# Kernel optimization log

Measured on AMD Instinct MI355X. Metric: run time of the kernel, lower is better.

## Reference

```python
import jax, jax.numpy as jnp
import numpy as np

B, M, D = 4, 2048, 1024


def setup_inputs() -> dict:
    key = jax.random.key(0)
    k1, k2, k3, k4 = jax.random.split(key, 4)
    x = jax.random.normal(k1, (B, M, D), dtype=jnp.float32)
    scale = 0.02
    wq = jax.random.normal(k2, (D, D), dtype=jnp.float32) * scale
    wk = jax.random.normal(k3, (D, D), dtype=jnp.float32) * scale
    wv = jax.random.normal(k4, (D, D), dtype=jnp.float32) * scale
    return {"x": x, "wq": wq, "wk": wk, "wv": wv}


def _rope_tables(m, d):
    # Faithful to source: phi = 10000 ** (-2*(i-1)/d)  (note the (i-1), incl. i=0)
    i = jnp.arange(d // 2, dtype=jnp.float32)
    phi = jnp.power(10000.0, -2.0 * (i - 1.0) / d)  # [d/2]
    pos = jnp.arange(m, dtype=jnp.float32)
    ang = pos[:, None] * phi[None, :]  # [m, d/2]
    return jnp.cos(ang), jnp.sin(ang)


def _apply_rope(t, cos, sin):
    # Original does t[pos] @ R[pos] (row-vector times rotation matrix):
    #   out_even =  t_even*cos + t_odd*sin
    #   out_odd  = -t_even*sin + t_odd*cos
    te = t[..., 0::2]  # [b, m, d/2]
    to = t[..., 1::2]
    oe = te * cos + to * sin
    oo = -te * sin + to * cos
    return jnp.stack([oe, oo], axis=-1).reshape(t.shape)


def reference(x, wq, wk, wv):
    b, m, d = x.shape
    q = x @ wq.T
    k = x @ wk.T
    v = x @ wv.T
    cos, sin = _rope_tables(m, d)
    qr = _apply_rope(q, cos, sin)
    kr = _apply_rope(k, cos, sin)
    # causal SDPA (dropout disabled for deterministic reference)
    scores = jnp.einsum('bqd,bkd->bqk', qr, kr) / jnp.sqrt(jnp.float32(d))
    causal = jnp.tril(jnp.ones((m, m), dtype=bool))
    scores = jnp.where(causal[None, :, :], scores, jnp.finfo(scores.dtype).min)
    attn = jax.nn.softmax(scores, axis=-1)
    return jnp.einsum('bqk,bkd->bqd', attn, v)
```

## Files before the change

### kernel.cpp

```cpp
#include <hip/hip_runtime.h>
#include <hip/hip_bf16.h>
#include <math.h>


typedef __bf16 bf16x8 __attribute__((ext_vector_type(8)));
typedef float  f32x4  __attribute__((ext_vector_type(4)));

__device__ __forceinline__ ushort f2bf(float f) {
    __hip_bfloat16 h = __float2bfloat16(f);
    return *reinterpret_cast<ushort*>(&h);
}

__device__ __forceinline__ void async_load16(const ushort* g, ushort* l) {
    __builtin_amdgcn_global_load_lds(
        (const __attribute__((address_space(1))) void*)g,
        (__attribute__((address_space(3))) void*)l, 16, 0, 0);
}

__global__ __launch_bounds__(256) void cvt_all_kernel(
    const float* __restrict__ x,  const float* __restrict__ wq,
    const float* __restrict__ wk, const float* __restrict__ wv,
    ushort* __restrict__ xb, ushort* __restrict__ wqb,
    ushort* __restrict__ wkb, ushort* __restrict__ wvb,
    float2* __restrict__ cs)
{
    const int t = blockIdx.y;
    if (t == 4) {
        const int idx = blockIdx.x * 256 + threadIdx.x;
        if (idx < 2048 * 512) {
            const int pos = idx >> 9, i = idx & 511;
            const float phi = powf(10000.0f, -2.0f * ((float)i - 1.0f) / 1024.0f);
            float s, c;
            sincosf((float)pos * phi, &s, &c);
            cs[idx] = make_float2(c, s);
        }
        return;
    }
    const float* in  = (t == 0) ? x  : (t == 1) ? wq  : (t == 2) ? wk  : wv;
    ushort*      out = (t == 0) ? xb : (t == 1) ? wqb : (t == 2) ? wkb : wvb;
    const int n4 = (t == 0) ? 2097152 : 262144;
    int i = blockIdx.x * blockDim.x + threadIdx.x;
    if (i < n4) {
        float4 f = ((const float4*)in)[i];
        ushort4 o;
        o.x = f2bf(f.x); o.y = f2bf(f.y); o.z = f2bf(f.z); o.w = f2bf(f.w);
        ((ushort4*)out)[i] = o;
    }
}

__device__ __forceinline__ void gemm128_core_sb(
    const ushort* __restrict__ A, const ushort* __restrict__ B,
    int lda, int ldb, int m0, int n0, int kIters,
    ushort* As, ushort* Bs, f32x4 acc[4][4])
{
    const int tid  = threadIdx.x;
    const int lane = tid & 63, wave = tid >> 6;
    const int wm = (wave >> 1) * 64, wn = (wave & 1) * 64;
    const int quad = lane >> 4, l16 = lane & 15;
    const int srow = lane >> 2, c = lane & 3;
    const int rr   = wave * 32 + srow;
    const int cc   = c ^ ((rr >> 1) & 3);
    const int scol = cc * 8;

    const ushort* ag0 = A + (size_t)(m0 + rr) * lda + scol;
    const ushort* bg0 = B + (size_t)(n0 + rr) * ldb + scol;
    const ushort* ag1 = ag0 + (size_t)16 * lda;
    const ushort* bg1 = bg0 + (size_t)16 * ldb;
    ushort* la0 = As + (wave * 32) * 32;
    ushort* la1 = la0 + 16 * 32;
    ushort* lb0 = Bs + (wave * 32) * 32;
    ushort* lb1 = lb0 + 16 * 32;

    for (int kt = 0; kt < kIters; ++kt) {
        const int k0 = kt * 32;
        async_load16(ag0 + k0, la0);
        async_load16(ag1 + k0, la1);
        async_load16(bg0 + k0, lb0);
        async_load16(bg1 + k0, lb1);
        __syncthreads();
        bf16x8 aF[4], bF[4];
#pragma unroll
        for (int i = 0; i < 4; ++i) {
            const int r = wm + i * 16 + l16;
            aF[i] = *(const bf16x8*)(As + r * 32 + ((quad ^ ((r >> 1) & 3)) * 8));
        }
#pragma unroll
        for (int j = 0; j < 4; ++j) {
            const int r = wn + j * 16 + l16;
            bF[j] = *(const bf16x8*)(Bs + r * 32 + ((quad ^ ((r >> 1) & 3)) * 8));
        }
#pragma unroll
        for (int i = 0; i < 4; ++i)
#pragma unroll
            for (int j = 0; j < 4; ++j)
                acc[i][j] = __builtin_amdgcn_mfma_f32_16x16x32_bf16(aF[i], bF[j], acc[i][j], 0, 0, 0);
        __syncthreads();
    }
}

__device__ __forceinline__ void gemm128_core_db(
    const ushort* __restrict__ A, const ushort* __restrict__ B,
    int lda, int ldb, int m0, int n0, int kIters,
    ushort* As, ushort* Bs, f32x4 acc[4][4])
{
    const int tid  = threadIdx.x;
    const int lane = tid & 63, wave = tid >> 6;
    const int wm = (wave >> 1) * 64, wn = (wave & 1) * 64;
    const int quad = lane >> 4, l16 = lane & 15;
    const int srow = lane >> 2, c = lane & 3;
    const int rr   = wave * 32 + srow;
    const int cc   = c ^ ((rr >> 1) & 3);
    const int scol = cc * 8;

    const ushort* ag0 = A + (size_t)(m0 + rr) * lda + scol;
    const ushort* bg0 = B + (size_t)(n0 + rr) * ldb + scol;
    const ushort* ag1 = ag0 + (size_t)16 * lda;
    const ushort* bg1 = bg0 + (size_t)16 * ldb;
    const int lofs = (wave * 32) * 32;

    async_load16(ag0, As + lofs);
    async_load16(ag1, As + lofs + 16 * 32);
    async_load16(bg0, Bs + lofs);
    async_load16(bg1, Bs + lofs + 16 * 32);
    __syncthreads();

    int cur = 0;
    for (int kt = 0; kt < kIters; ++kt) {
        if (kt + 1 < kIters) {
            const int k1 = (kt + 1) * 32;
            const int nb = (cur ^ 1) * 4096;
            async_load16(ag0 + k1, As + nb + lofs);
            async_load16(ag1 + k1, As + nb + lofs + 16 * 32);
            async_load16(bg0 + k1, Bs + nb + lofs);
            async_load16(bg1 + k1, Bs + nb + lofs + 16 * 32);
        }
        const ushort* as = As + cur * 4096;
        const ushort* bs = Bs + cur * 4096;
        bf16x8 aF[4], bF[4];
#pragma unroll
        for (int i = 0; i < 4; ++i) {
            const int r = wm + i * 16 + l16;
            aF[i] = *(const bf16x8*)(as + r * 32 + ((quad ^ ((r >> 1) & 3)) * 8));
        }
#pragma unroll
        for (int j = 0; j < 4; ++j) {
            const int r = wn + j * 16 + l16;
            bF[j] = *(const bf16x8*)(bs + r * 32 + ((quad ^ ((r >> 1) & 3)) * 8));
        }
#pragma unroll
        for (int i = 0; i < 4; ++i)
#pragma unroll
            for (int j = 0; j < 4; ++j)
                acc[i][j] = __builtin_amdgcn_mfma_f32_16x16x32_bf16(aF[i], bF[j], acc[i][j], 0, 0, 0);
        __syncthreads();
        cur ^= 1;
    }
}

#define ACC_INIT4(acc) \
    _Pragma("unroll") for (int i = 0; i < 4; ++i) \
    _Pragma("unroll") for (int j = 0; j < 4; ++j) \
    _Pragma("unroll") for (int r = 0; r < 4; ++r) acc[i][j][r] = 0.0f;

__global__ __launch_bounds__(256) void qkv_rope_kernel(
    const ushort* __restrict__ xb, const ushort* __restrict__ wq,
    const ushort* __restrict__ wk, const ushort* __restrict__ wv,
    const float2* __restrict__ cs,
    ushort* __restrict__ Qr, ushort* __restrict__ Kr, ushort* __restrict__ VT)
{
    __shared__ __attribute__((aligned(16))) ushort As[128 * 32];
    __shared__ __attribute__((aligned(16))) ushort Bs[128 * 32];
    const int m0 = blockIdx.x * 128;
    const int n0 = blockIdx.y * 128;
    const int z  = blockIdx.z;
    const ushort* W = (z == 0) ? wq : (z == 1) ? wk : wv;

    f32x4 acc[4][4];
    ACC_INIT4(acc)
    gemm128_core_sb(xb, W, 1024, 1024, m0, n0, 32, As, Bs, acc);

    const int lane = threadIdx.x & 63, wave = threadIdx.x >> 6;
    const int wm = (wave >> 1) * 64, wn = (wave & 1) * 64;
    const int quad = lane >> 4, l16 = lane & 15;

    if (z < 2) {
        ushort* out = (z == 0) ? Qr : Kr;
#pragma unroll
        for (int j = 0; j < 4; ++j) {
            const int n = n0 + wn + j * 16 + l16;
            const int iidx = n >> 1;
            const bool odd = n & 1;
#pragma unroll
            for (int i = 0; i < 4; ++i) {
                const int mbase = m0 + wm + i * 16 + quad * 4;
                const int pos0  = mbase & 2047;
                const float2* csp = cs + (size_t)pos0 * 512 + iidx;
#pragma unroll
                for (int r = 0; r < 4; ++r) {
                    const float2 sc = csp[(size_t)r * 512];
                    float v = acc[i][j][r];
                    float p = __shfl_xor(v, 1);
                    float o = odd ? (v * sc.x - p * sc.y) : (v * sc.x + p * sc.y);
                    out[(size_t)(mbase + r) * 1024 + n] = f2bf(o);
                }
            }
        }
    } else {
#pragma unroll
        for (int i = 0; i < 4; ++i) {
            const int mbase = m0 + wm + i * 16 + quad * 4;
            const int b = mbase >> 11, pos0 = mbase & 2047;
#pragma unroll
            for (int j = 0; j < 4; ++j) {
                const int n = n0 + wn + j * 16 + l16;
                ushort4 o;
                o.x = f2bf(acc[i][j][0]); o.y = f2bf(acc[i][j][1]);
                o.z = f2bf(acc[i][j][2]); o.w = f2bf(acc[i][j][3]);
                *(ushort4*)(VT + ((size_t)b * 1024 + n) * 2048 + pos0) = o;
            }
        }
    }
}

__global__ __launch_bounds__(256) void scores_kernel(
    const ushort* __restrict__ Qr, const ushort* __restrict__ Kr,
    float* __restrict__ S)
{
    const int m0 = blockIdx.x * 128;
    const int n0 = blockIdx.y * 128;
    if (n0 > m0 + 127) return;
    const int b = blockIdx.z;
    __shared__ __attribute__((aligned(16))) ushort As[2 * 128 * 32];
    __shared__ __attribute__((aligned(16))) ushort Bs[2 * 128 * 32];
    const ushort* A = Qr + (size_t)b * 2048 * 1024;
    const ushort* B = Kr + (size_t)b * 2048 * 1024;
    float* Sb = S + (size_t)b * 2048 * 2048;

    f32x4 acc[4][4];
    ACC_INIT4(acc)
    gemm128_core_db(A, B, 1024, 1024, m0, n0, 32, As, Bs, acc);

    const int lane = threadIdx.x & 63, wave = threadIdx.x >> 6;
    const int wm = (wave >> 1) * 64, wn = (wave & 1) * 64;
    const int quad = lane >> 4, l16 = lane & 15;
#pragma unroll
    for (int i = 0; i < 4; ++i)
#pragma unroll
        for (int j = 0; j < 4; ++j) {
            const int n = n0 + wn + j * 16 + l16;
#pragma unroll
            for (int r = 0; r < 4; ++r) {
                const int m = m0 + wm + i * 16 + quad * 4 + r;
                Sb[(size_t)m * 2048 + n] = acc[i][j][r] * 0.03125f;
            }
        }
}

__global__ __launch_bounds__(256) void softmax_kernel(
    const float* __restrict__ S, ushort* __restrict__ P)
{
    __shared__ float red[4];
    const int row = blockIdx.x, tid = threadIdx.x, b = blockIdx.y;
    const int lane = tid & 63, wave = tid >> 6;
    const float* s = S + ((size_t)b * 2048 + row) * 2048;
    ushort*      p = P + ((size_t)b * 2048 + row) * 2048;
    const int nvalid = row + 1;
    const int wlimit = (row & ~127) + 128;
    const int j0 = tid * 8;

    float v[8] = {0.0f, 0.0f, 0.0f, 0.0f, 0.0f, 0.0f, 0.0f, 0.0f};
    if (j0 < nvalid) {
        float4 f0 = *(const float4*)(s + j0);
        v[0]=f0.x; v[1]=f0.y; v[2]=f0.z; v[3]=f0.w;
    }
    if (j0 + 4 < nvalid) {
        float4 f1 = *(const float4*)(s + j0 + 4);
        v[4]=f1.x; v[5]=f1.y; v[6]=f1.z; v[7]=f1.w;
    }

    float mx = -3.402823466e38f;
#pragma unroll
    for (int u = 0; u < 8; ++u) if (j0 + u < nvalid) mx = fmaxf(mx, v[u]);
#pragma unroll
    for (int d = 1; d < 64; d <<= 1) mx = fmaxf(mx, __shfl_xor(mx, d));
    if (lane == 0) red[wave] = mx;
    __syncthreads();
    mx = fmaxf(fmaxf(red[0], red[1]), fmaxf(red[2], red[3]));

    float sum = 0.0f;
#pragma unroll
    for (int u = 0; u < 8; ++u) {
        v[u] = (j0 + u < nvalid) ? __expf(v[u] - mx) : 0.0f;
        sum += v[u];
    }
#pragma unroll
    for (int d = 1; d < 64; d <<= 1) sum += __shfl_xor(sum, d);
    __syncthreads();
    if (lane == 0) red[wave] = sum;
    __syncthreads();
    const float inv = 1.0f / (red[0] + red[1] + red[2] + red[3]);

    if (j0 < wlimit) {
        ushort o[8];
#pragma unroll
        for (int u = 0; u < 8; ++u) o[u] = f2bf(v[u] * inv);
        *(int4*)(p + j0) = *(const int4*)o;
    }
}

__global__ __launch_bounds__(256) void pv_kernel(
    const ushort* __restrict__ P, const ushort* __restrict__ VT,
    float* __restrict__ out)
{
    __shared__ __attribute__((aligned(16))) ushort As[2 * 128 * 32];
    __shared__ __attribute__((aligned(16))) ushort Bs[2 * 128 * 32];
    const int x  = blockIdx.x;
    const int mt = (x & 1) ? (15 - (x >> 1)) : (x >> 1);
    const int m0 = mt * 128;
    const int n0 = blockIdx.y * 128;
    const int b  = blockIdx.z;
    const ushort* A = P + (size_t)b * 2048 * 2048;
    const ushort* B = VT + (size_t)b * 1024 * 2048;
    const int kIters = (m0 + 128) / 32;

    f32x4 acc[4][4];
    ACC_INIT4(acc)
    gemm128_core_db(A, B, 2048, 2048, m0, n0, kIters, As, Bs, acc);

    const int lane = threadIdx.x & 63, wave = threadIdx.x >> 6;
    const int wm = (wave >> 1) * 64, wn = (wave & 1) * 64;
    const int quad = lane >> 4, l16 = lane & 15;
#pragma unroll
    for (int i = 0; i < 4; ++i)
#pragma unroll
        for (int j = 0; j < 4; ++j) {
            const int n = n0 + wn + j * 16 + l16;
#pragma unroll
            for (int r = 0; r < 4; ++r) {
                const int m = m0 + wm + i * 16 + quad * 4 + r;
                out[((size_t)b * 2048 + m) * 1024 + n] = acc[i][j][r];
            }
        }
}

extern "C" void kernel_launch(void* const* d_in, const int* in_sizes, int n_in,
                              void* d_out, int out_size, void* d_ws, size_t ws_size,
                              hipStream_t stream) {
    const float* x  = (const float*)d_in[0];
    const float* wq = (const float*)d_in[1];
    const float* wk = (const float*)d_in[2];
    const float* wv = (const float*)d_in[3];

    const size_t MiB = 1024 * 1024;
    char* ws = (char*)d_ws;
    ushort* xb  = (ushort*)(ws);
    ushort* wqb = (ushort*)(ws +  16 * MiB);
    ushort* wkb = (ushort*)(ws +  18 * MiB);
    ushort* wvb = (ushort*)(ws +  20 * MiB);
    ushort* Qr  = (ushort*)(ws +  22 * MiB);
    ushort* Kr  = (ushort*)(ws +  38 * MiB);
    ushort* VT  = (ushort*)(ws +  54 * MiB);
    float*  S   = (float* )(ws +  70 * MiB);
    ushort* P   = (ushort*)(ws + 134 * MiB);
    float2* cs  = (float2*)(ws + 166 * MiB);
    float*  out = (float*)d_out;

    cvt_all_kernel <<<dim3(8192, 5),   256, 0, stream>>>(x, wq, wk, wv, xb, wqb, wkb, wvb, cs);
    qkv_rope_kernel<<<dim3(64, 8, 3),  256, 0, stream>>>(xb, wqb, wkb, wvb, cs, Qr, Kr, VT);
    scores_kernel  <<<dim3(16, 16, 4), 256, 0, stream>>>(Qr, Kr, S);
    softmax_kernel <<<dim3(2048, 4),   256, 0, stream>>>(S, P);
    pv_kernel      <<<dim3(16, 8, 4),  256, 0, stream>>>(P, VT, out);
}
```

Baseline: 274.7 us.

## Split-K the scores GEMM into two halves and widen QKV GEMM K-tile to 64

```diff
diff --git a/kernel.cpp b/kernel.cpp
--- a/kernel.cpp
+++ b/kernel.cpp
@@ -48,7 +48,7 @@
     }
 }
 
-__device__ __forceinline__ void gemm128_core_sb(
+__device__ __forceinline__ void gemm128_core_sb64(
     const ushort* __restrict__ A, const ushort* __restrict__ B,
     int lda, int ldb, int m0, int n0, int kIters,
     ushort* As, ushort* Bs, f32x4 acc[4][4])
@@ -57,43 +57,38 @@
     const int lane = tid & 63, wave = tid >> 6;
     const int wm = (wave >> 1) * 64, wn = (wave & 1) * 64;
     const int quad = lane >> 4, l16 = lane & 15;
-    const int srow = lane >> 2, c = lane & 3;
-    const int rr   = wave * 32 + srow;
-    const int cc   = c ^ ((rr >> 1) & 3);
-    const int scol = cc * 8;
-
-    const ushort* ag0 = A + (size_t)(m0 + rr) * lda + scol;
-    const ushort* bg0 = B + (size_t)(n0 + rr) * ldb + scol;
-    const ushort* ag1 = ag0 + (size_t)16 * lda;
-    const ushort* bg1 = bg0 + (size_t)16 * ldb;
-    ushort* la0 = As + (wave * 32) * 32;
-    ushort* la1 = la0 + 16 * 32;
-    ushort* lb0 = Bs + (wave * 32) * 32;
-    ushort* lb1 = lb0 + 16 * 32;
+    const int srow8 = lane >> 3;
+    const int gchk  = (lane & 7) ^ srow8;
+    const ushort* ag = A + (size_t)(m0 + wave * 32 + srow8) * lda + gchk * 8;
+    const ushort* bg = B + (size_t)(n0 + wave * 32 + srow8) * ldb + gchk * 8;
+    const int p0 = quad ^ (l16 & 7);
 
     for (int kt = 0; kt < kIters; ++kt) {
-        const int k0 = kt * 32;
-        async_load16(ag0 + k0, la0);
-        async_load16(ag1 + k0, la1);
-        async_load16(bg0 + k0, lb0);
-        async_load16(bg1 + k0, lb1);
+        const int k0 = kt * 64;
+#pragma unroll
+        for (int s = 0; s < 4; ++s) {
+            async_load16(ag + k0 + (size_t)(s * 8) * lda,
+                         As + (wave * 32 + s * 8) * 64);
+            async_load16(bg + k0 + (size_t)(s * 8) * ldb,
+                         Bs + (wave * 32 + s * 8) * 64);
+        }
         __syncthreads();
-        bf16x8 aF[4], bF[4];
-#pragma unroll
-        for (int i = 0; i < 4; ++i) {
-            const int r = wm + i * 16 + l16;
-            aF[i] = *(const bf16x8*)(As + r * 32 + ((quad ^ ((r >> 1) & 3)) * 8));
-        }
-#pragma unroll
-        for (int j = 0; j < 4; ++j) {
-            const int r = wn + j * 16 + l16;
-            bF[j] = *(const bf16x8*)(Bs + r * 32 + ((quad ^ ((r >> 1) & 3)) * 8));
-        }
-#pragma unroll
-        for (int i = 0; i < 4; ++i)
+#pragma unroll
+        for (int kk = 0; kk < 2; ++kk) {
+            const int poff = (p0 ^ (kk << 2)) * 8;
+            bf16x8 aF[4], bF[4];
+#pragma unroll
+            for (int i = 0; i < 4; ++i)
+                aF[i] = *(const bf16x8*)(As + (wm + i * 16 + l16) * 64 + poff);
 #pragma unroll
             for (int j = 0; j < 4; ++j)
-                acc[i][j] = __builtin_amdgcn_mfma_f32_16x16x32_bf16(aF[i], bF[j], acc[i][j], 0, 0, 0);
+                bF[j] = *(const bf16x8*)(Bs + (wn + j * 16 + l16) * 64 + poff);
+#pragma unroll
+            for (int i = 0; i < 4; ++i)
+#pragma unroll
+                for (int j = 0; j < 4; ++j)
+                    acc[i][j] = __builtin_amdgcn_mfma_f32_16x16x32_bf16(aF[i], bF[j], acc[i][j], 0, 0, 0);
+        }
         __syncthreads();
     }
 }
@@ -168,8 +163,8 @@
     const float2* __restrict__ cs,
     ushort* __restrict__ Qr, ushort* __restrict__ Kr, ushort* __restrict__ VT)
 {
-    __shared__ __attribute__((aligned(16))) ushort As[128 * 32];
-    __shared__ __attribute__((aligned(16))) ushort Bs[128 * 32];
+    __shared__ __attribute__((aligned(16))) ushort As[128 * 64];
+    __shared__ __attribute__((aligned(16))) ushort Bs[128 * 64];
     const int m0 = blockIdx.x * 128;
     const int n0 = blockIdx.y * 128;
     const int z  = blockIdx.z;
@@ -177,7 +172,7 @@
 
     f32x4 acc[4][4];
     ACC_INIT4(acc)
-    gemm128_core_sb(xb, W, 1024, 1024, m0, n0, 32, As, Bs, acc);
+    gemm128_core_sb64(xb, W, 1024, 1024, m0, n0, 16, As, Bs, acc);
 
     const int lane = threadIdx.x & 63, wave = threadIdx.x >> 6;
     const int wm = (wave >> 1) * 64, wn = (wave & 1) * 64;
@@ -224,21 +219,22 @@
 
 __global__ __launch_bounds__(256) void scores_kernel(
     const ushort* __restrict__ Qr, const ushort* __restrict__ Kr,
-    float* __restrict__ S)
+    float* __restrict__ S1, float* __restrict__ S2)
 {
     const int m0 = blockIdx.x * 128;
     const int n0 = blockIdx.y * 128;
     if (n0 > m0 + 127) return;
-    const int b = blockIdx.z;
+    const int b = blockIdx.z >> 1;
+    const int h = blockIdx.z & 1;
     __shared__ __attribute__((aligned(16))) ushort As[2 * 128 * 32];
     __shared__ __attribute__((aligned(16))) ushort Bs[2 * 128 * 32];
-    const ushort* A = Qr + (size_t)b * 2048 * 1024;
-    const ushort* B = Kr + (size_t)b * 2048 * 1024;
-    float* Sb = S + (size_t)b * 2048 * 2048;
+    const ushort* A = Qr + (size_t)b * 2048 * 1024 + h * 512;
+    const ushort* B = Kr + (size_t)b * 2048 * 1024 + h * 512;
+    float* Sb = (h ? S2 : S1) + (size_t)b * 2048 * 2048;
 
     f32x4 acc[4][4];
     ACC_INIT4(acc)
-    gemm128_core_db(A, B, 1024, 1024, m0, n0, 32, As, Bs, acc);
+    gemm128_core_db(A, B, 1024, 1024, m0, n0, 16, As, Bs, acc);
 
     const int lane = threadIdx.x & 63, wave = threadIdx.x >> 6;
     const int wm = (wave >> 1) * 64, wn = (wave & 1) * 64;
@@ -257,25 +253,29 @@
 }
 
 __global__ __launch_bounds__(256) void softmax_kernel(
-    const float* __restrict__ S, ushort* __restrict__ P)
+    const float* __restrict__ S1, const float* __restrict__ S2,
+    ushort* __restrict__ P)
 {
     __shared__ float red[4];
     const int row = blockIdx.x, tid = threadIdx.x, b = blockIdx.y;
     const int lane = tid & 63, wave = tid >> 6;
-    const float* s = S + ((size_t)b * 2048 + row) * 2048;
-    ushort*      p = P + ((size_t)b * 2048 + row) * 2048;
+    const float* s1 = S1 + ((size_t)b * 2048 + row) * 2048;
+    const float* s2 = S2 + ((size_t)b * 2048 + row) * 2048;
+    ushort*      p  = P  + ((size_t)b * 2048 + row) * 2048;
     const int nvalid = row + 1;
     const int wlimit = (row & ~127) + 128;
     const int j0 = tid * 8;
 
     float v[8] = {0.0f, 0.0f, 0.0f, 0.0f, 0.0f, 0.0f, 0.0f, 0.0f};
     if (j0 < nvalid) {
-        float4 f0 = *(const float4*)(s + j0);
-        v[0]=f0.x; v[1]=f0.y; v[2]=f0.z; v[3]=f0.w;
+        float4 a = *(const float4*)(s1 + j0);
+        float4 c = *(const float4*)(s2 + j0);
+        v[0]=a.x+c.x; v[1]=a.y+c.y; v[2]=a.z+c.z; v[3]=a.w+c.w;
     }
     if (j0 + 4 < nvalid) {
-        float4 f1 = *(const float4*)(s + j0 + 4);
-        v[4]=f1.x; v[5]=f1.y; v[6]=f1.z; v[7]=f1.w;
+        float4 a = *(const float4*)(s1 + j0 + 4);
+        float4 c = *(const float4*)(s2 + j0 + 4);
+        v[4]=a.x+c.x; v[5]=a.y+c.y; v[6]=a.z+c.z; v[7]=a.w+c.w;
     }
 
     float mx = -3.402823466e38f;
@@ -360,14 +360,15 @@
     ushort* Qr  = (ushort*)(ws +  22 * MiB);
     ushort* Kr  = (ushort*)(ws +  38 * MiB);
     ushort* VT  = (ushort*)(ws +  54 * MiB);
-    float*  S   = (float* )(ws +  70 * MiB);
+    float*  S1  = (float* )(ws +  70 * MiB);
     ushort* P   = (ushort*)(ws + 134 * MiB);
     float2* cs  = (float2*)(ws + 166 * MiB);
+    float*  S2  = (float* )(ws + 174 * MiB);
     float*  out = (float*)d_out;
 
     cvt_all_kernel <<<dim3(8192, 5),   256, 0, stream>>>(x, wq, wk, wv, xb, wqb, wkb, wvb, cs);
     qkv_rope_kernel<<<dim3(64, 8, 3),  256, 0, stream>>>(xb, wqb, wkb, wvb, cs, Qr, Kr, VT);
-    scores_kernel  <<<dim3(16, 16, 4), 256, 0, stream>>>(Qr, Kr, S);
-    softmax_kernel <<<dim3(2048, 4),   256, 0, stream>>>(S, P);
+    scores_kernel  <<<dim3(16, 16, 8), 256, 0, stream>>>(Qr, Kr, S1, S2);
+    softmax_kernel <<<dim3(2048, 4),   256, 0, stream>>>(S1, S2, P);
     pv_kernel      <<<dim3(16, 8, 4),  256, 0, stream>>>(P, VT, out);
 }
```

Result: no change. 277.1 us (+0.9%).
